# Kernel optimization log

Measured on AMD Instinct MI355X. Metric: run time of the kernel, lower is better.

Reference implementation:

```python
import jax, jax.numpy as jnp
import numpy as np

N_USERS = 100000
N_ITEMS = 50000
N_NODES = N_USERS + N_ITEMS
D = 64
N_LAYERS = 3
POP_BINS = 10
NNZ = 2000000
BATCH = 256
BIAS_SCALE = 1.0


def setup_inputs() -> dict:
    key = jax.random.key(0)
    ks = jax.random.split(key, 16)
    std = 0.01
    inp = {
        "user_emb": jax.random.normal(ks[0], (N_USERS, D), jnp.float32) * std,
        "item_emb": jax.random.normal(ks[1], (N_ITEMS, D), jnp.float32) * std,
        "user_bias": jnp.zeros((N_USERS, 1), jnp.float32),
        "item_bias": jnp.zeros((N_ITEMS, 1), jnp.float32),
        "pop_emb": jax.random.normal(ks[2], (POP_BINS, D), jnp.float32) * std,
        "uW1": jax.random.normal(ks[3], (D, D), jnp.float32) / np.sqrt(D),
        "ub1": jnp.zeros((D,), jnp.float32),
        "uW2": jax.random.normal(ks[4], (D, D), jnp.float32) / np.sqrt(D),
        "ub2": jnp.zeros((D,), jnp.float32),
        "iW1": jax.random.normal(ks[5], (D, D), jnp.float32) / np.sqrt(D),
        "ib1": jnp.zeros((D,), jnp.float32),
        "iW2": jax.random.normal(ks[6], (D, D), jnp.float32) / np.sqrt(D),
        "ib2": jnp.zeros((D,), jnp.float32),
        "gW1": jax.random.normal(ks[7], (2 * D, D), jnp.float32) / np.sqrt(2 * D),
        "gb1": jnp.zeros((D,), jnp.float32),
        "gW2": jax.random.normal(ks[8], (D, 1), jnp.float32) / np.sqrt(D),
        "gb2": jnp.zeros((1,), jnp.float32),
        "adj_vals": jax.random.uniform(ks[9], (NNZ,), jnp.float32),
        "adj_rows": jax.random.randint(ks[10], (NNZ,), 0, N_NODES, jnp.int32),
        "adj_cols": jax.random.randint(ks[11], (NNZ,), 0, N_NODES, jnp.int32),
        "item_pop_bins": jax.random.randint(ks[12], (N_ITEMS,), 0, POP_BINS, jnp.int32),
        "users": jax.random.randint(ks[13], (BATCH,), 0, N_USERS, jnp.int32),
    }
    return inp


def _spmm(vals, rows, cols, E):
    # sparse (N x N) @ E  via gather + segment-sum
    msgs = vals[:, None] * E[cols]          # [nnz, d]
    return jax.ops.segment_sum(msgs, rows, num_segments=N_NODES)


def _mlp2(x, W1, b1, W2, b2):
    return jax.nn.relu(x @ W1 + b1) @ W2 + b2


def reference(user_emb, item_emb, user_bias, item_bias, pop_emb,
              uW1, ub1, uW2, ub2, iW1, ib1, iW2, ib2,
              gW1, gb1, gW2, gb2,
              adj_vals, adj_rows, adj_cols, item_pop_bins, users):
    # ---- computer(): LightGCN propagation with uniform layer weights ----
    emb = jnp.concatenate([user_emb, item_emb], axis=0)   # [N, d]
    w = 1.0 / (N_LAYERS + 1)
    out = emb * w
    cur = emb
    for _ in range(N_LAYERS):
        cur = _spmm(adj_vals, adj_rows, adj_cols, cur)
        out = out + cur * w
    all_users, all_items = out[:N_USERS], out[N_USERS:]

    # ---- popularity-gated item fusion ----
    p_vec = pop_emb[item_pop_bins]                         # [n_items, d]
    gate_in = jnp.concatenate([all_items, p_vec], axis=-1)
    z = jax.nn.sigmoid(_mlp2(gate_in, gW1, gb1, gW2, gb2)) # [n_items, 1]
    items_fused = (1.0 - z) * all_items + z * p_vec

    # ---- two-tower scoring over all items ----
    U = _mlp2(all_users[users], uW1, ub1, uW2, ub2)        # [B, d]
    I = _mlp2(items_fused, iW1, ib1, iW2, ib2)             # [n_items, d]
    scores = U @ I.T                                        # [B, n_items]
    scores = scores + user_bias[users] * BIAS_SCALE + (item_bias.T) * BIAS_SCALE
    return scores
```

## Files before the change

kernel.cpp:

```cpp
#include <hip/hip_runtime.h>
#include <hip/hip_fp16.h>

#define N_USERS 100000
#define N_ITEMS 50000
#define N_NODES 150000
#define D 64
#define NNZ 2000000
#define BATCH 256
#define POP_BINS 10

#define BSH 9
#define NB2 293
#define CAP 8192
#define P1_EPB 4096
#define P1_BLOCKS 489

#define ST_P 130
#define MAXC 7

__global__ __launch_bounds__(256) void k_p1(const int* __restrict__ rows,
                                            const int* __restrict__ cols,
                                            const float* __restrict__ vals,
                                            int* __restrict__ bcur,
                                            uint2* __restrict__ gstage) {
  __shared__ int cnt[NB2];
  __shared__ int gbase[NB2];
  int t = threadIdx.x;
  for (int i = t; i < NB2; i += 256) cnt[i] = 0;
  __syncthreads();
  int base = blockIdx.x * P1_EPB;
  for (int i = 0; i < 16; i++) {
    int e = base + i * 256 + t;
    if (e < NNZ) atomicAdd(&cnt[rows[e] >> BSH], 1);
  }
  __syncthreads();
  for (int i = t; i < NB2; i += 256) {
    int c = cnt[i];
    gbase[i] = c ? atomicAdd(&bcur[i], c) : 0;
    cnt[i] = 0;
  }
  __syncthreads();
  for (int i = 0; i < 16; i++) {
    int e = base + i * 256 + t;
    if (e < NNZ) {
      int r = rows[e];
      int b = r >> BSH;
      int rank = atomicAdd(&cnt[b], 1);
      unsigned key = ((unsigned)(r & 511) << 18) | (unsigned)cols[e];
      gstage[(size_t)b * CAP + gbase[b] + rank] =
          make_uint2(key, __float_as_uint(vals[e]));
    }
  }
}

__global__ __launch_bounds__(256) void k_p2(const int* __restrict__ bcur,
                                            const uint2* __restrict__ gstage,
                                            uint2* __restrict__ epack,
                                            int* __restrict__ rowbeg,
                                            int* __restrict__ rowend,
                                            int* __restrict__ gcursor) {
  __shared__ int cnt[512];
  __shared__ int off[512];
  __shared__ int s[256];
  __shared__ int gbs;
  __shared__ uint2 buf[CAP];
  int b = blockIdx.x, t = threadIdx.x;
  int n = bcur[b];
  const uint2* gs = gstage + (size_t)b * CAP;
  if (t == 0) gbs = atomicAdd(gcursor, n);
  cnt[t] = 0;
  cnt[t + 256] = 0;
  __syncthreads();
  for (int j = t; j < n; j += 256)
    atomicAdd(&cnt[gs[j].x >> 18], 1);
  __syncthreads();
  int c0 = cnt[2 * t], c1 = cnt[2 * t + 1];
  s[t] = c0 + c1;
  __syncthreads();
  for (int o = 1; o < 256; o <<= 1) {
    int x = (t >= o) ? s[t - o] : 0;
    __syncthreads();
    s[t] += x;
    __syncthreads();
  }
  int ex = t ? s[t - 1] : 0;
  off[2 * t] = ex;
  off[2 * t + 1] = ex + c0;
  int base = gbs;
  int gr = (b << BSH) + 2 * t;
  if (gr < N_NODES) { rowbeg[gr] = base + ex; rowend[gr] = base + ex + c0; }
  if (gr + 1 < N_NODES) { rowbeg[gr + 1] = base + ex + c0; rowend[gr + 1] = base + ex + c0 + c1; }
  __syncthreads();
  for (int j = t; j < n; j += 256) {
    uint2 ed = gs[j];
    int lr = ed.x >> 18;
    int pos = atomicAdd(&off[lr], 1);
    buf[pos] = make_uint2(ed.x & 0x3FFFFu, ed.y);
  }
  __syncthreads();
  for (int j = t; j < n; j += 256) epack[base + j] = buf[j];
}

__global__ __launch_bounds__(256) void k_flags(const int* __restrict__ users,
                                               int* __restrict__ uflag,
                                               int* __restrict__ ulist,
                                               int* __restrict__ ucnt) {
  int u = users[threadIdx.x];
  int old = atomicOr(&uflag[u >> 5], 1 << (u & 31));
  if (!((old >> (u & 31)) & 1)) {
    int p = atomicAdd(ucnt, 1);
    ulist[p] = u;
  }
}

__global__ __launch_bounds__(256) void k_cvt(const float* __restrict__ ue,
                                             const float* __restrict__ ie,
                                             __half* __restrict__ Eh) {
  int t = blockIdx.x * 256 + threadIdx.x;
  if (t >= 2400000) return;
  size_t fo = (size_t)t * 4;
  const float* src = (fo < (size_t)N_USERS * 64) ? ue + fo
                                                 : ie + (fo - (size_t)N_USERS * 64);
  float4 v = *(const float4*)src;
  __half2* dst = (__half2*)(Eh + fo);
  dst[0] = __floats2half2_rn(v.x, v.y);
  dst[1] = __floats2half2_rn(v.z, v.w);
}

#define SPMM_DEEP(TBL)                                                        \
  int n = end - beg;                                                          \
  int nc = (n + 3) >> 2;                                                      \
  if (nc > MAXC) nc = MAXC;                                                   \
  uint2 ed[MAXC];                                                             \
  _Pragma("unroll")                                                           \
  for (int c = 0; c < MAXC; c++) {                                            \
    if (c < nc) {                                                             \
      int jj = beg + 4 * c + q;                                               \
      int jc = jj < end ? jj : end - 1;                                       \
      ed[c] = epack[jc];                                                      \
    }                                                                         \
  }                                                                           \
  uint2 rg[MAXC]; float rv[MAXC];                                             \
  _Pragma("unroll")                                                           \
  for (int c = 0; c < MAXC; c++) {                                            \
    if (c < nc) {                                                             \
      int jj = beg + 4 * c + q;                                               \
      rv[c] = (jj < end) ? __uint_as_float(ed[c].y) : 0.f;                    \
      rg[c] = *(const uint2*)(TBL + (size_t)ed[c].x * 64 + 4 * p);            \
    }                                                                         \
  }                                                                           \
  float a0 = 0.f, a1 = 0.f, a2 = 0.f, a3 = 0.f;                               \
  _Pragma("unroll")                                                           \
  for (int c = 0; c < MAXC; c++) {                                            \
    if (c < nc) {                                                             \
      float2 lo = __half22float2(*(const __half2*)&rg[c].x);                  \
      float2 hi = __half22float2(*(const __half2*)&rg[c].y);                  \
      a0 += rv[c] * lo.x; a1 += rv[c] * lo.y;                                 \
      a2 += rv[c] * hi.x; a3 += rv[c] * hi.y;                                 \
    }                                                                         \
  }                                                                           \
  for (int j = beg + 4 * MAXC; j < end; j += 4) {   \
    int jj = j + q;                                                           \
    int jc = jj < end ? jj : end - 1;                                         \
    uint2 e = epack[jc];                                                      \
    float v = (jj < end) ? __uint_as_float(e.y) : 0.f;                        \
    uint2 r = *(const uint2*)(TBL + (size_t)e.x * 64 + 4 * p);                \
    float2 lo = __half22float2(*(const __half2*)&r.x);                        \
    float2 hi = __half22float2(*(const __half2*)&r.y);                        \
    a0 += v * lo.x; a1 += v * lo.y; a2 += v * hi.x; a3 += v * hi.y;           \
  }                                                                           \
  a0 += __shfl_xor(a0, 16, 64); a0 += __shfl_xor(a0, 32, 64);                 \
  a1 += __shfl_xor(a1, 16, 64); a1 += __shfl_xor(a1, 32, 64);                 \
  a2 += __shfl_xor(a2, 16, 64); a2 += __shfl_xor(a2, 32, 64);                 \
  a3 += __shfl_xor(a3, 16, 64); a3 += __shfl_xor(a3, 32, 64);

__global__ __launch_bounds__(256) void k_spmm1(const int* __restrict__ rowbeg,
                                               const int* __restrict__ rowend,
                                               const uint2* __restrict__ epack,
                                               const float* __restrict__ ue,
                                               const float* __restrict__ ie,
                                               const __half* __restrict__ Eh0,
                                               const int* __restrict__ uflag,
                                               __half* __restrict__ EoutH,
                                               float* __restrict__ Oacc) {
  int wave = blockIdx.x * 4 + (threadIdx.x >> 6);
  int row = __builtin_amdgcn_readfirstlane(wave);
  if (row >= N_NODES) return;
  int lane = threadIdx.x & 63;
  int p = lane & 15, q = lane >> 4;
  int beg = rowbeg[row];
  int end = rowend[row];
  SPMM_DEEP(Eh0)
  if (q == 0) {
    __half2* eo = (__half2*)(EoutH + (size_t)row * 64 + 4 * p);
    eo[0] = __floats2half2_rn(a0, a1);
    eo[1] = __floats2half2_rn(a2, a3);
    bool need = (row >= N_USERS) || (((uflag[row >> 5] >> (row & 31)) & 1) != 0);
    if (need) {
      const float* srow = (row < N_USERS) ? ue + (size_t)row * 64
                                          : ie + (size_t)(row - N_USERS) * 64;
      float4 sv = *(const float4*)(srow + 4 * p);
      *(float4*)(Oacc + (size_t)row * 64 + 4 * p) =
          make_float4(0.25f * (sv.x + a0), 0.25f * (sv.y + a1),
                      0.25f * (sv.z + a2), 0.25f * (sv.w + a3));
    }
  }
}

__global__ __launch_bounds__(256) void k_spmm2h(const int* __restrict__ rowbeg,
                                                const int* __restrict__ rowend,
                                                const uint2* __restrict__ epack,
                                                const __half* __restrict__ Ein,
                                                const int* __restrict__ uflag,
                                                __half* __restrict__ EoutH,
                                                float* __restrict__ Oacc) {
  int wave = blockIdx.x * 4 + (threadIdx.x >> 6);
  int row = __builtin_amdgcn_readfirstlane(wave);
  if (row >= N_NODES) return;
  int lane = threadIdx.x & 63;
  int p = lane & 15, q = lane >> 4;
  int beg = rowbeg[row];
  int end = rowend[row];
  SPMM_DEEP(Ein)
  if (q == 0) {
    __half2* eo = (__half2*)(EoutH + (size_t)row * 64 + 4 * p);
    eo[0] = __floats2half2_rn(a0, a1);
    eo[1] = __floats2half2_rn(a2, a3);
    if (row >= N_USERS || (((uflag[row >> 5] >> (row & 31)) & 1) != 0)) {
      float4* op = (float4*)(Oacc + (size_t)row * 64 + 4 * p);
      float4 cur = *op;
      *op = make_float4(cur.x + 0.25f * a0, cur.y + 0.25f * a1,
                        cur.z + 0.25f * a2, cur.w + 0.25f * a3);
    }
  }
}

__global__ __launch_bounds__(256) void k_spmm3h(const int* __restrict__ rowbeg,
                                                const int* __restrict__ rowend,
                                                const uint2* __restrict__ epack,
                                                const __half* __restrict__ Ein,
                                                const int* __restrict__ ulist,
                                                const int* __restrict__ ucnt,
                                                float* __restrict__ Oacc) {
  int w = blockIdx.x * 4 + (threadIdx.x >> 6);
  int row;
  if (w < N_ITEMS) {
    row = N_USERS + w;
  } else {
    int k = w - N_ITEMS;
    if (k >= ucnt[0]) return;
    row = ulist[k];
  }
  row = __builtin_amdgcn_readfirstlane(row);
  int lane = threadIdx.x & 63;
  int p = lane & 15, q = lane >> 4;
  int beg = rowbeg[row];
  int end = rowend[row];
  SPMM_DEEP(Ein)
  if (q == 0) {
    float4* op = (float4*)(Oacc + (size_t)row * 64 + 4 * p);
    float4 cur = *op;
    *op = make_float4(cur.x + 0.25f * a0, cur.y + 0.25f * a1,
                      cur.z + 0.25f * a2, cur.w + 0.25f * a3);
  }
}

__global__ __launch_bounds__(256) void k_pw(const float* __restrict__ pop,
                                            const float* __restrict__ gW1,
                                            const float* __restrict__ iW1,
                                            float* __restrict__ hp,
                                            float* __restrict__ pp1) {
  for (int idx = threadIdx.x; idx < 2 * POP_BINS * 64; idx += 256) {
    int q = idx;
    bool second = q >= POP_BINS * 64;
    if (second) q -= POP_BINS * 64;
    int b = q >> 6, o = q & 63;
    float s = 0.f;
    if (!second) {
      for (int k = 0; k < 64; k++) s += pop[b * 64 + k] * gW1[(64 + k) * 64 + o];
      hp[q] = s;
    } else {
      for (int k = 0; k < 64; k++) s += pop[b * 64 + k] * iW1[k * 64 + o];
      pp1[q] = s;
    }
  }
}

__global__ __launch_bounds__(256) void k_user(const float* __restrict__ Oacc,
                                              const int* __restrict__ users,
                                              const float* __restrict__ ubias,
                                              const float* __restrict__ uW1,
                                              const float* __restrict__ ub1,
                                              const float* __restrict__ uW2,
                                              const float* __restrict__ ub2,
                                              float* __restrict__ Ut) {
  int ub = blockIdx.x * 4 + (threadIdx.x >> 6);
  int lane = threadIdx.x & 63;
  int u = users[ub];
  float x = Oacc[(size_t)u * 64 + lane];
  float h = ub1[lane];
#pragma unroll
  for (int k = 0; k < 64; k++)
    h = fmaf(__shfl(x, k, 64), uW1[k * 64 + lane], h);
  h = h > 0.f ? h : 0.f;
  float o = ub2[lane];
#pragma unroll
  for (int k = 0; k < 64; k++)
    o = fmaf(__shfl(h, k, 64), uW2[k * 64 + lane], o);
  Ut[lane * 256 + ub] = o;
  if (lane == 0) Ut[64 * 256 + ub] = ubias[u];
}

__global__ __launch_bounds__(256) void k_gemm1z(const float* __restrict__ Oacc,
                                                const float* __restrict__ gW1,
                                                const float* __restrict__ iW1,
                                                const int* __restrict__ bins,
                                                const float* __restrict__ hp,
                                                const float* __restrict__ pp1,
                                                const float* __restrict__ gb1,
                                                const float* __restrict__ gW2,
                                                const float* __restrict__ gb2,
                                                const float* __restrict__ ib1,
                                                float* __restrict__ H1) {
  __shared__ float Is[64 * ST_P];
  __shared__ float Bs[64 * 128];
  __shared__ float zp[128][9];
  __shared__ float zs[128];
  int tid = threadIdx.x;
  int i0 = blockIdx.x * 128;
  {
    int c4 = tid & 15, r0 = tid >> 4;
#pragma unroll
    for (int s = 0; s < 8; s++) {
      int r = r0 + s * 16;
      int it = i0 + r;
      float4 v = make_float4(0.f, 0.f, 0.f, 0.f);
      if (it < N_ITEMS) v = *(const float4*)(Oacc + (size_t)(N_USERS + it) * 64 + c4 * 4);
      Is[(c4 * 4 + 0) * ST_P + r] = v.x;
      Is[(c4 * 4 + 1) * ST_P + r] = v.y;
      Is[(c4 * 4 + 2) * ST_P + r] = v.z;
      Is[(c4 * 4 + 3) * ST_P + r] = v.w;
    }
  }
  for (int idx = tid; idx < 64 * 128; idx += 256) {
    int k = idx >> 7, o = idx & 127;
    Bs[idx] = (o < 64) ? gW1[k * 64 + o] : iW1[k * 64 + (o - 64)];
  }
  __syncthreads();
  int tx = tid & 15, ty = tid >> 4;
  float acc[8][8];
#pragma unroll
  for (int a = 0; a < 8; a++)
#pragma unroll
    for (int b = 0; b < 8; b++) acc[a][b] = 0.f;
  const float* ip = Is + tx * 8;
  const float* wp = Bs + ty * 8;
#pragma unroll 2
  for (int k = 0; k < 64; k++) {
    float4 iv0 = *(const float4*)(ip + k * ST_P);
    float4 iv1 = *(const float4*)(ip + k * ST_P + 4);
    float4 wv0 = *(const float4*)(wp + k * 128);
    float4 wv1 = *(const float4*)(wp + k * 128 + 4);
    float iv[8] = {iv0.x, iv0.y, iv0.z, iv0.w, iv1.x, iv1.y, iv1.z, iv1.w};
    float wv[8] = {wv0.x, wv0.y, wv0.z, wv0.w, wv1.x, wv1.y, wv1.z, wv1.w};
#pragma unroll
    for (int a = 0; a < 8; a++)
#pragma unroll
      for (int b = 0; b < 8; b++) acc[a][b] += iv[a] * wv[b];
  }
  int ibase = i0 + tx * 8;
  if (ty < 8) {
    int o0 = ty * 8;
#pragma unroll
    for (int a = 0; a < 8; a++) {
      int it = ibase + a;
      float p = 0.f;
      if (it < N_ITEMS) {
        int bin = bins[it];
        const float* hpr = hp + bin * 64 + o0;
#pragma unroll
        for (int b = 0; b < 8; b++) {
          float g = acc[a][b] + hpr[b] + gb1[o0 + b];
          g = g > 0.f ? g : 0.f;
          p += g * gW2[o0 + b];
        }
      }
      zp[tx * 8 + a][ty] = p;
    }
  }
  __syncthreads();
  if (tid < 128) {
    float s = gb2[0];
#pragma unroll
    for (int k = 0; k < 8; k++) s += zp[tid][k];
    zs[tid] = 1.f / (1.f + expf(-s));
  }
  __syncthreads();
  if (ty >= 8) {
    int o0 = (ty - 8) * 8;
#pragma unroll
    for (int a = 0; a < 8; a++) {
      int it = ibase + a;
      if (it < N_ITEMS) {
        float z = zs[tx * 8 + a];
        int bin = bins[it];
        const float* ppr = pp1 + bin * 64 + o0;
        float h[8];
#pragma unroll
        for (int b = 0; b < 8; b++) {
          float v = (1.f - z) * acc[a][b] + z * ppr[b] + ib1[o0 + b];
          h[b] = v > 0.f ? v : 0.f;
        }
        *(float4*)(H1 + (size_t)it * 64 + o0) = make_float4(h[0], h[1], h[2], h[3]);
        *(float4*)(H1 + (size_t)it * 64 + o0 + 4) = make_float4(h[4], h[5], h[6], h[7]);
      }
    }
  }
}

__global__ __launch_bounds__(256) void k_gemm2(const float* __restrict__ H1,
                                               const float* __restrict__ iW2,
                                               const float* __restrict__ ib2,
                                               float* __restrict__ I) {
  __shared__ float Is[64 * ST_P];
  __shared__ float Bs[64 * 64];
  int tid = threadIdx.x;
  int i0 = blockIdx.x * 128;
  {
    int c4 = tid & 15, r0 = tid >> 4;
#pragma unroll
    for (int s = 0; s < 8; s++) {
      int r = r0 + s * 16;
      int it = i0 + r;
      float4 v = make_float4(0.f, 0.f, 0.f, 0.f);
      if (it < N_ITEMS) v = *(const float4*)(H1 + (size_t)it * 64 + c4 * 4);
      Is[(c4 * 4 + 0) * ST_P + r] = v.x;
      Is[(c4 * 4 + 1) * ST_P + r] = v.y;
      Is[(c4 * 4 + 2) * ST_P + r] = v.z;
      Is[(c4 * 4 + 3) * ST_P + r] = v.w;
    }
  }
  for (int idx = tid; idx < 64 * 64; idx += 256) Bs[idx] = iW2[idx];
  __syncthreads();
  int tx = tid & 15, ty = tid >> 4;
  float acc[8][4];
#pragma unroll
  for (int a = 0; a < 8; a++)
#pragma unroll
    for (int b = 0; b < 4; b++) acc[a][b] = 0.f;
  const float* ip = Is + tx * 8;
  const float* wp = Bs + ty * 4;
#pragma unroll 2
  for (int k = 0; k < 64; k++) {
    float4 iv0 = *(const float4*)(ip + k * ST_P);
    float4 iv1 = *(const float4*)(ip + k * ST_P + 4);
    float4 wv = *(const float4*)(wp + k * 64);
    float iv[8] = {iv0.x, iv0.y, iv0.z, iv0.w, iv1.x, iv1.y, iv1.z, iv1.w};
    float wvv[4] = {wv.x, wv.y, wv.z, wv.w};
#pragma unroll
    for (int a = 0; a < 8; a++)
#pragma unroll
      for (int b = 0; b < 4; b++) acc[a][b] += iv[a] * wvv[b];
  }
  int ibase = i0 + tx * 8;
  int oc = ty * 4;
  float b0 = ib2[oc], b1 = ib2[oc + 1], b2 = ib2[oc + 2], b3 = ib2[oc + 3];
#pragma unroll
  for (int a = 0; a < 8; a++) {
    int it = ibase + a;
    if (it < N_ITEMS) {
      float4 s0 = make_float4(acc[a][0] + b0, acc[a][1] + b1,
                              acc[a][2] + b2, acc[a][3] + b3);
      *(float4*)(I + (size_t)it * 64 + oc) = s0;
    }
  }
}

__global__ __launch_bounds__(256) void k_scores(const float* __restrict__ I,
                                                const float* __restrict__ Ut,
                                                const float* __restrict__ item_bias,
                                                float* __restrict__ out) {
  __shared__ float Is[64 * ST_P];
  __shared__ float Us[64 * 128];
  int tid = threadIdx.x;
  int i0 = blockIdx.x * 128;
  int ubase = blockIdx.y * 128;
  {
    int c4 = tid & 15, r0 = tid >> 4;
#pragma unroll
    for (int s = 0; s < 8; s++) {
      int r = r0 + s * 16;
      int it = i0 + r;
      float4 v = make_float4(0.f, 0.f, 0.f, 0.f);
      if (it < N_ITEMS) v = *(const float4*)(I + (size_t)it * 64 + c4 * 4);
      Is[(c4 * 4 + 0) * ST_P + r] = v.x;
      Is[(c4 * 4 + 1) * ST_P + r] = v.y;
      Is[(c4 * 4 + 2) * ST_P + r] = v.z;
      Is[(c4 * 4 + 3) * ST_P + r] = v.w;
    }
  }
  {
    int u4 = tid & 31, k0 = tid >> 5;
#pragma unroll
    for (int s = 0; s < 8; s++) {
      int k = k0 + s * 8;
      float4 v = *(const float4*)(Ut + k * 256 + ubase + u4 * 4);
      *(float4*)(Us + k * 128 + u4 * 4) = v;
    }
  }
  __syncthreads();
  int tx = tid & 15;
  int ty = tid >> 4;
  float acc[8][8];
#pragma unroll
  for (int a = 0; a < 8; a++)
#pragma unroll
    for (int b = 0; b < 8; b++) acc[a][b] = 0.f;
  const float* ip = Is + tx * 8;
  const float* up = Us + ty * 8;
#pragma unroll 2
  for (int k = 0; k < 64; k++) {
    float4 iv0 = *(const float4*)(ip + k * ST_P);
    float4 iv1 = *(const float4*)(ip + k * ST_P + 4);
    float4 uv0 = *(const float4*)(up + k * 128);
    float4 uv1 = *(const float4*)(up + k * 128 + 4);
    float iv[8] = {iv0.x, iv0.y, iv0.z, iv0.w, iv1.x, iv1.y, iv1.z, iv1.w};
    float uv[8] = {uv0.x, uv0.y, uv0.z, uv0.w, uv1.x, uv1.y, uv1.z, uv1.w};
#pragma unroll
    for (int a = 0; a < 8; a++)
#pragma unroll
      for (int b = 0; b < 8; b++) acc[a][b] += iv[a] * uv[b];
  }
  int ibase = i0 + tx * 8;
  float ib[8];
#pragma unroll
  for (int a = 0; a < 8; a++)
    ib[a] = (ibase + a < N_ITEMS) ? item_bias[ibase + a] : 0.f;
#pragma unroll
  for (int bb = 0; bb < 8; bb++) {
    int bu = ubase + ty * 8 + bb;
    float ubias = Ut[64 * 256 + bu];
    float* orow = out + (size_t)bu * N_ITEMS + ibase;
    if (ibase + 7 < N_ITEMS) {
      float4 s0 = make_float4(acc[0][bb] + ubias + ib[0], acc[1][bb] + ubias + ib[1],
                              acc[2][bb] + ubias + ib[2], acc[3][bb] + ubias + ib[3]);
      float4 s1 = make_float4(acc[4][bb] + ubias + ib[4], acc[5][bb] + ubias + ib[5],
                              acc[6][bb] + ubias + ib[6], acc[7][bb] + ubias + ib[7]);
      *(float4*)orow = s0;
      *(float4*)(orow + 4) = s1;
    } else {
#pragma unroll
      for (int a = 0; a < 8; a++)
        if (ibase + a < N_ITEMS) orow[a] = acc[a][bb] + ubias + ib[a];
    }
  }
}

extern "C" void kernel_launch(void* const* d_in, const int* in_sizes, int n_in,
                              void* d_out, int out_size, void* d_ws, size_t ws_size,
                              hipStream_t stream) {
  const float* user_emb  = (const float*)d_in[0];
  const float* item_emb  = (const float*)d_in[1];
  const float* user_bias = (const float*)d_in[2];
  const float* item_bias = (const float*)d_in[3];
  const float* pop_emb   = (const float*)d_in[4];
  const float* uW1 = (const float*)d_in[5];
  const float* ub1 = (const float*)d_in[6];
  const float* uW2 = (const float*)d_in[7];
  const float* ub2 = (const float*)d_in[8];
  const float* iW1 = (const float*)d_in[9];
  const float* ib1 = (const float*)d_in[10];
  const float* iW2 = (const float*)d_in[11];
  const float* ib2 = (const float*)d_in[12];
  const float* gW1 = (const float*)d_in[13];
  const float* gb1 = (const float*)d_in[14];
  const float* gW2 = (const float*)d_in[15];
  const float* gb2 = (const float*)d_in[16];
  const float* adj_vals = (const float*)d_in[17];
  const int* adj_rows = (const int*)d_in[18];
  const int* adj_cols = (const int*)d_in[19];
  const int* bins  = (const int*)d_in[20];
  const int* users = (const int*)d_in[21];
  float* out = (float*)d_out;

  float* ws = (float*)d_ws;
  float* Oacc = ws;
  float* bufA = ws + 9600000;
  float* bufB = ws + 19200000;
  uint2* epack = (uint2*)(ws + 28800000);
  int* rowbeg = (int*)(ws + 32800000);
  int* rowend = (int*)(ws + 32950000);
  int* uflag  = (int*)(ws + 33100000);
  int* ucnt   = (int*)(ws + 33103125);
  int* ulist  = (int*)(ws + 33103130);
  float* Ut   = ws + 33104000;
  float* hp   = ws + 33121000;
  float* pp1  = ws + 33122000;
  int* bcur   = (int*)(ws + 33123000);
  int* gcursor = (int*)(ws + 33123293);
  uint2* gstage = (uint2*)bufB;
  __half* Eh0 = (__half*)bufA;
  __half* E1h = (__half*)(bufA + 4800000);
  __half* E2h = (__half*)bufB;
  float* H1 = bufA + 6400000;
  float* I  = bufB;

  hipMemsetAsync(bcur, 0, 294 * sizeof(int), stream);
  hipMemsetAsync(uflag, 0, 3126 * sizeof(int), stream);
  k_cvt<<<9375, 256, 0, stream>>>(user_emb, item_emb, Eh0);
  k_p1<<<P1_BLOCKS, 256, 0, stream>>>(adj_rows, adj_cols, adj_vals, bcur, gstage);
  k_p2<<<NB2, 256, 0, stream>>>(bcur, gstage, epack, rowbeg, rowend, gcursor);
  k_flags<<<1, 256, 0, stream>>>(users, uflag, ulist, ucnt);

  k_spmm1<<<37500, 256, 0, stream>>>(rowbeg, rowend, epack, user_emb, item_emb, Eh0, uflag, E1h, Oacc);
  k_spmm2h<<<37500, 256, 0, stream>>>(rowbeg, rowend, epack, E1h, uflag, E2h, Oacc);
  k_spmm3h<<<12564, 256, 0, stream>>>(rowbeg, rowend, epack, E2h, ulist, ucnt, Oacc);

  k_pw<<<1, 256, 0, stream>>>(pop_emb, gW1, iW1, hp, pp1);
  k_user<<<64, 256, 0, stream>>>(Oacc, users, user_bias, uW1, ub1, uW2, ub2, Ut);
  k_gemm1z<<<391, 256, 0, stream>>>(Oacc, gW1, iW1, bins, hp, pp1, gb1, gW2, gb2, ib1, H1);
  k_gemm2<<<391, 256, 0, stream>>>(H1, iW2, ib2, I);
  k_scores<<<dim3(391, 2), 256, 0, stream>>>(I, Ut, item_bias, out);
}
```

Measured before the change: 505.6 us.

## Fuse small kernels, merge item MLP GEMMs, simplify SpMM gather loop

Folds the user-flag kernel into an extra block of the bucket-sort kernel and the pop-weight kernel into an extra block of the fp16 conversion kernel. It also merges the two item-MLP GEMMs so H1 stays in shared memory instead of going through global memory. The scores kernel now loops over both user halves per block rather than using a 2D grid. The SpMM gather replaces the deep register-prefetch loop with a simpler 2-way unrolled loop, and the workspace layout is rearranged so a single memset clears the flags and counters. Together these cut launch overhead and global traffic, at the risk of less memory-level parallelism in the SpMM and lower parallelism in the scores kernel.

```diff
diff --git a/kernel.cpp b/kernel.cpp
--- a/kernel.cpp
+++ b/kernel.cpp
@@ -16,7 +16,6 @@
 #define P1_BLOCKS 489
 
 #define ST_P 130
-#define MAXC 7
 
 __global__ __launch_bounds__(256) void k_p1(const int* __restrict__ rows,
                                             const int* __restrict__ cols,
@@ -58,13 +57,26 @@
                                             uint2* __restrict__ epack,
                                             int* __restrict__ rowbeg,
                                             int* __restrict__ rowend,
-                                            int* __restrict__ gcursor) {
+                                            int* __restrict__ gcursor,
+                                            const int* __restrict__ users,
+                                            int* __restrict__ uflag,
+                                            int* __restrict__ ulist,
+                                            int* __restrict__ ucnt) {
+  int b = blockIdx.x, t = threadIdx.x;
+  if (b == NB2) {
+    int u = users[t];
+    int old = atomicOr(&uflag[u >> 5], 1 << (u & 31));
+    if (!((old >> (u & 31)) & 1)) {
+      int p = atomicAdd(ucnt, 1);
+      ulist[p] = u;
+    }
+    return;
+  }
   __shared__ int cnt[512];
   __shared__ int off[512];
   __shared__ int s[256];
   __shared__ int gbs;
   __shared__ uint2 buf[CAP];
-  int b = blockIdx.x, t = threadIdx.x;
   int n = bcur[b];
   const uint2* gs = gstage + (size_t)b * CAP;
   if (t == 0) gbs = atomicAdd(gcursor, n);
@@ -101,23 +113,33 @@
   for (int j = t; j < n; j += 256) epack[base + j] = buf[j];
 }
 
-__global__ __launch_bounds__(256) void k_flags(const int* __restrict__ users,
-                                               int* __restrict__ uflag,
-                                               int* __restrict__ ulist,
-                                               int* __restrict__ ucnt) {
-  int u = users[threadIdx.x];
-  int old = atomicOr(&uflag[u >> 5], 1 << (u & 31));
-  if (!((old >> (u & 31)) & 1)) {
-    int p = atomicAdd(ucnt, 1);
-    ulist[p] = u;
-  }
-}
-
-__global__ __launch_bounds__(256) void k_cvt(const float* __restrict__ ue,
-                                             const float* __restrict__ ie,
-                                             __half* __restrict__ Eh) {
-  int t = blockIdx.x * 256 + threadIdx.x;
-  if (t >= 2400000) return;
+__global__ __launch_bounds__(256) void k_prep(const float* __restrict__ ue,
+                                              const float* __restrict__ ie,
+                                              __half* __restrict__ Eh,
+                                              const float* __restrict__ pop,
+                                              const float* __restrict__ gW1,
+                                              const float* __restrict__ iW1,
+                                              float* __restrict__ hp,
+                                              float* __restrict__ pp1) {
+  int b = blockIdx.x;
+  if (b == 9375) {
+    for (int idx = threadIdx.x; idx < 2 * POP_BINS * 64; idx += 256) {
+      int q = idx;
+      bool second = q >= POP_BINS * 64;
+      if (second) q -= POP_BINS * 64;
+      int bb = q >> 6, o = q & 63;
+      float s = 0.f;
+      if (!second) {
+        for (int k = 0; k < 64; k++) s += pop[bb * 64 + k] * gW1[(64 + k) * 64 + o];
+        hp[q] = s;
+      } else {
+        for (int k = 0; k < 64; k++) s += pop[bb * 64 + k] * iW1[k * 64 + o];
+        pp1[q] = s;
+      }
+    }
+    return;
+  }
+  int t = b * 256 + threadIdx.x;
   size_t fo = (size_t)t * 4;
   const float* src = (fo < (size_t)N_USERS * 64) ? ue + fo
                                                  : ie + (fo - (size_t)N_USERS * 64);
@@ -127,41 +149,25 @@
   dst[1] = __floats2half2_rn(v.z, v.w);
 }
 
-#define SPMM_DEEP(TBL)                                                        \
-  int n = end - beg;                                                          \
-  int nc = (n + 3) >> 2;                                                      \
-  if (nc > MAXC) nc = MAXC;                                                   \
-  uint2 ed[MAXC];                                                             \
-  _Pragma("unroll")                                                           \
-  for (int c = 0; c < MAXC; c++) {                                            \
-    if (c < nc) {                                                             \
-      int jj = beg + 4 * c + q;                                               \
-      int jc = jj < end ? jj : end - 1;                                       \
-      ed[c] = epack[jc];                                                      \
-    }                                                                         \
+#define SPMM_QW_BODY(TBL)                                                     \
+  float a0 = 0.f, a1 = 0.f, a2 = 0.f, a3 = 0.f;                               \
+  int j = beg;                                                                \
+  for (; j + 7 < end; j += 8) {                                               \
+    uint2 ea = epack[j + q];                                                  \
+    uint2 eb = epack[j + 4 + q];                                              \
+    uint2 ra = *(const uint2*)(TBL + (size_t)ea.x * 64 + 4 * p);              \
+    uint2 rb = *(const uint2*)(TBL + (size_t)eb.x * 64 + 4 * p);              \
+    float va = __uint_as_float(ea.y), vb = __uint_as_float(eb.y);             \
+    float2 la = __half22float2(*(const __half2*)&ra.x);                       \
+    float2 ha = __half22float2(*(const __half2*)&ra.y);                       \
+    float2 lb = __half22float2(*(const __half2*)&rb.x);                       \
+    float2 hb = __half22float2(*(const __half2*)&rb.y);                       \
+    a0 += va * la.x; a1 += va * la.y; a2 += va * ha.x; a3 += va * ha.y;       \
+    a0 += vb * lb.x; a1 += vb * lb.y; a2 += vb * hb.x; a3 += vb * hb.y;       \
   }                                                                           \
-  uint2 rg[MAXC]; float rv[MAXC];                                             \
-  _Pragma("unroll")                                                           \
-  for (int c = 0; c < MAXC; c++) {                                            \
-    if (c < nc) {                                                             \
-      int jj = beg + 4 * c + q;                                               \
-      rv[c] = (jj < end) ? __uint_as_float(ed[c].y) : 0.f;                    \
-      rg[c] = *(const uint2*)(TBL + (size_t)ed[c].x * 64 + 4 * p);            \
-    }                                                                         \
-  }                                                                           \
-  float a0 = 0.f, a1 = 0.f, a2 = 0.f, a3 = 0.f;                               \
-  _Pragma("unroll")                                                           \
-  for (int c = 0; c < MAXC; c++) {                                            \
-    if (c < nc) {                                                             \
-      float2 lo = __half22float2(*(const __half2*)&rg[c].x);                  \
-      float2 hi = __half22float2(*(const __half2*)&rg[c].y);                  \
-      a0 += rv[c] * lo.x; a1 += rv[c] * lo.y;                                 \
-      a2 += rv[c] * hi.x; a3 += rv[c] * hi.y;                                 \
-    }                                                                         \
-  }                                                                           \
-  for (int j = beg + 4 * MAXC; j < end; j += 4) {   \
+  for (; j < end; j += 4) {                                                   \
     int jj = j + q;                                                           \
-    int jc = jj < end ? jj : end - 1;                                         \
+    int jc = (jj < end) ? jj : end - 1;                                       \
     uint2 e = epack[jc];                                                      \
     float v = (jj < end) ? __uint_as_float(e.y) : 0.f;                        \
     uint2 r = *(const uint2*)(TBL + (size_t)e.x * 64 + 4 * p);                \
@@ -190,7 +196,7 @@
   int p = lane & 15, q = lane >> 4;
   int beg = rowbeg[row];
   int end = rowend[row];
-  SPMM_DEEP(Eh0)
+  SPMM_QW_BODY(Eh0)
   if (q == 0) {
     __half2* eo = (__half2*)(EoutH + (size_t)row * 64 + 4 * p);
     eo[0] = __floats2half2_rn(a0, a1);
@@ -221,7 +227,7 @@
   int p = lane & 15, q = lane >> 4;
   int beg = rowbeg[row];
   int end = rowend[row];
-  SPMM_DEEP(Ein)
+  SPMM_QW_BODY(Ein)
   if (q == 0) {
     __half2* eo = (__half2*)(EoutH + (size_t)row * 64 + 4 * p);
     eo[0] = __floats2half2_rn(a0, a1);
@@ -256,33 +262,12 @@
   int p = lane & 15, q = lane >> 4;
   int beg = rowbeg[row];
   int end = rowend[row];
-  SPMM_DEEP(Ein)
+  SPMM_QW_BODY(Ein)
   if (q == 0) {
     float4* op = (float4*)(Oacc + (size_t)row * 64 + 4 * p);
     float4 cur = *op;
     *op = make_float4(cur.x + 0.25f * a0, cur.y + 0.25f * a1,
                       cur.z + 0.25f * a2, cur.w + 0.25f * a3);
-  }
-}
-
-__global__ __launch_bounds__(256) void k_pw(const float* __restrict__ pop,
-                                            const float* __restrict__ gW1,
-                                            const float* __restrict__ iW1,
-                                            float* __restrict__ hp,
-                                            float* __restrict__ pp1) {
-  for (int idx = threadIdx.x; idx < 2 * POP_BINS * 64; idx += 256) {
-    int q = idx;
-    bool second = q >= POP_BINS * 64;
-    if (second) q -= POP_BINS * 64;
-    int b = q >> 6, o = q & 63;
-    float s = 0.f;
-    if (!second) {
-      for (int k = 0; k < 64; k++) s += pop[b * 64 + k] * gW1[(64 + k) * 64 + o];
-      hp[q] = s;
-    } else {
-      for (int k = 0; k < 64; k++) s += pop[b * 64 + k] * iW1[k * 64 + o];
-      pp1[q] = s;
-    }
   }
 }
 
@@ -311,7 +296,7 @@
   if (lane == 0) Ut[64 * 256 + ub] = ubias[u];
 }
 
-__global__ __launch_bounds__(256) void k_gemm1z(const float* __restrict__ Oacc,
+__global__ __launch_bounds__(256) void k_gemm12(const float* __restrict__ Oacc,
                                                 const float* __restrict__ gW1,
                                                 const float* __restrict__ iW1,
                                                 const int* __restrict__ bins,
@@ -321,7 +306,9 @@
                                                 const float* __restrict__ gW2,
                                                 const float* __restrict__ gb2,
                                                 const float* __restrict__ ib1,
-                                                float* __restrict__ H1) {
+                                                const float* __restrict__ iW2,
+                                                const float* __restrict__ ib2,
+                                                float* __restrict__ I) {
   __shared__ float Is[64 * ST_P];
   __shared__ float Bs[64 * 128];
   __shared__ float zp[128][9];
@@ -353,20 +340,22 @@
   for (int a = 0; a < 8; a++)
 #pragma unroll
     for (int b = 0; b < 8; b++) acc[a][b] = 0.f;
-  const float* ip = Is + tx * 8;
-  const float* wp = Bs + ty * 8;
+  {
+    const float* ip = Is + tx * 8;
+    const float* wp = Bs + ty * 8;
 #pragma unroll 2
-  for (int k = 0; k < 64; k++) {
-    float4 iv0 = *(const float4*)(ip + k * ST_P);
-    float4 iv1 = *(const float4*)(ip + k * ST_P + 4);
-    float4 wv0 = *(const float4*)(wp + k * 128);
-    float4 wv1 = *(const float4*)(wp + k * 128 + 4);
-    float iv[8] = {iv0.x, iv0.y, iv0.z, iv0.w, iv1.x, iv1.y, iv1.z, iv1.w};
-    float wv[8] = {wv0.x, wv0.y, wv0.z, wv0.w, wv1.x, wv1.y, wv1.z, wv1.w};
-#pragma unroll
-    for (int a = 0; a < 8; a++)
-#pragma unroll
-      for (int b = 0; b < 8; b++) acc[a][b] += iv[a] * wv[b];
+    for (int k = 0; k < 64; k++) {
+      float4 iv0 = *(const float4*)(ip + k * ST_P);
+      float4 iv1 = *(const float4*)(ip + k * ST_P + 4);
+      float4 wv0 = *(const float4*)(wp + k * 128);
+      float4 wv1 = *(const float4*)(wp + k * 128 + 4);
+      float iv[8] = {iv0.x, iv0.y, iv0.z, iv0.w, iv1.x, iv1.y, iv1.z, iv1.w};
+      float wv[8] = {wv0.x, wv0.y, wv0.z, wv0.w, wv1.x, wv1.y, wv1.z, wv1.w};
+#pragma unroll
+      for (int a = 0; a < 8; a++)
+#pragma unroll
+        for (int b = 0; b < 8; b++) acc[a][b] += iv[a] * wv[b];
+    }
   }
   int ibase = i0 + tx * 8;
   if (ty < 8) {
@@ -401,76 +390,48 @@
 #pragma unroll
     for (int a = 0; a < 8; a++) {
       int it = ibase + a;
-      if (it < N_ITEMS) {
-        float z = zs[tx * 8 + a];
-        int bin = bins[it];
-        const float* ppr = pp1 + bin * 64 + o0;
-        float h[8];
-#pragma unroll
-        for (int b = 0; b < 8; b++) {
-          float v = (1.f - z) * acc[a][b] + z * ppr[b] + ib1[o0 + b];
-          h[b] = v > 0.f ? v : 0.f;
-        }
-        *(float4*)(H1 + (size_t)it * 64 + o0) = make_float4(h[0], h[1], h[2], h[3]);
-        *(float4*)(H1 + (size_t)it * 64 + o0 + 4) = make_float4(h[4], h[5], h[6], h[7]);
+      int item = tx * 8 + a;
+      float z = zs[item];
+      int bin = (it < N_ITEMS) ? bins[it] : 0;
+      const float* ppr = pp1 + bin * 64 + o0;
+#pragma unroll
+      for (int b = 0; b < 8; b++) {
+        float v = (1.f - z) * acc[a][b] + z * ppr[b] + ib1[o0 + b];
+        Is[(o0 + b) * ST_P + item] = v > 0.f ? v : 0.f;
       }
     }
   }
-}
-
-__global__ __launch_bounds__(256) void k_gemm2(const float* __restrict__ H1,
-                                               const float* __restrict__ iW2,
-                                               const float* __restrict__ ib2,
-                                               float* __restrict__ I) {
-  __shared__ float Is[64 * ST_P];
-  __shared__ float Bs[64 * 64];
-  int tid = threadIdx.x;
-  int i0 = blockIdx.x * 128;
+  for (int idx = tid; idx < 64 * 64; idx += 256) Bs[idx] = iW2[idx];
+  __syncthreads();
+  float acc2[8][4];
+#pragma unroll
+  for (int a = 0; a < 8; a++)
+#pragma unroll
+    for (int b = 0; b < 4; b++) acc2[a][b] = 0.f;
   {
-    int c4 = tid & 15, r0 = tid >> 4;
-#pragma unroll
-    for (int s = 0; s < 8; s++) {
-      int r = r0 + s * 16;
-      int it = i0 + r;
-      float4 v = make_float4(0.f, 0.f, 0.f, 0.f);
-      if (it < N_ITEMS) v = *(const float4*)(H1 + (size_t)it * 64 + c4 * 4);
-      Is[(c4 * 4 + 0) * ST_P + r] = v.x;
-      Is[(c4 * 4 + 1) * ST_P + r] = v.y;
-      Is[(c4 * 4 + 2) * ST_P + r] = v.z;
-      Is[(c4 * 4 + 3) * ST_P + r] = v.w;
-    }
-  }
-  for (int idx = tid; idx < 64 * 64; idx += 256) Bs[idx] = iW2[idx];
-  __syncthreads();
-  int tx = tid & 15, ty = tid >> 4;
-  float acc[8][4];
-#pragma unroll
-  for (int a = 0; a < 8; a++)
-#pragma unroll
-    for (int b = 0; b < 4; b++) acc[a][b] = 0.f;
-  const float* ip = Is + tx * 8;
-  const float* wp = Bs + ty * 4;
+    const float* ip = Is + tx * 8;
+    const float* wp = Bs + ty * 4;
 #pragma unroll 2
-  for (int k = 0; k < 64; k++) {
-    float4 iv0 = *(const float4*)(ip + k * ST_P);
-    float4 iv1 = *(const float4*)(ip + k * ST_P + 4);
-    float4 wv = *(const float4*)(wp + k * 64);
-    float iv[8] = {iv0.x, iv0.y, iv0.z, iv0.w, iv1.x, iv1.y, iv1.z, iv1.w};
-    float wvv[4] = {wv.x, wv.y, wv.z, wv.w};
-#pragma unroll
-    for (int a = 0; a < 8; a++)
-#pragma unroll
-      for (int b = 0; b < 4; b++) acc[a][b] += iv[a] * wvv[b];
-  }
-  int ibase = i0 + tx * 8;
+    for (int k = 0; k < 64; k++) {
+      float4 iv0 = *(const float4*)(ip + k * ST_P);
+      float4 iv1 = *(const float4*)(ip + k * ST_P + 4);
+      float4 wv = *(const float4*)(wp + k * 64);
+      float iv[8] = {iv0.x, iv0.y, iv0.z, iv0.w, iv1.x, iv1.y, iv1.z, iv1.w};
+      float wvv[4] = {wv.x, wv.y, wv.z, wv.w};
+#pragma unroll
+      for (int a = 0; a < 8; a++)
+#pragma unroll
+        for (int b = 0; b < 4; b++) acc2[a][b] += iv[a] * wvv[b];
+    }
+  }
   int oc = ty * 4;
   float b0 = ib2[oc], b1 = ib2[oc + 1], b2 = ib2[oc + 2], b3 = ib2[oc + 3];
 #pragma unroll
   for (int a = 0; a < 8; a++) {
     int it = ibase + a;
     if (it < N_ITEMS) {
-      float4 s0 = make_float4(acc[a][0] + b0, acc[a][1] + b1,
-                              acc[a][2] + b2, acc[a][3] + b3);
+      float4 s0 = make_float4(acc2[a][0] + b0, acc2[a][1] + b1,
+                              acc2[a][2] + b2, acc2[a][3] + b3);
       *(float4*)(I + (size_t)it * 64 + oc) = s0;
     }
   }
@@ -484,7 +445,6 @@
   __shared__ float Us[64 * 128];
   int tid = threadIdx.x;
   int i0 = blockIdx.x * 128;
-  int ubase = blockIdx.y * 128;
   {
     int c4 = tid & 15, r0 = tid >> 4;
 #pragma unroll
@@ -499,59 +459,63 @@
       Is[(c4 * 4 + 3) * ST_P + r] = v.w;
     }
   }
-  {
-    int u4 = tid & 31, k0 = tid >> 5;
-#pragma unroll
-    for (int s = 0; s < 8; s++) {
-      int k = k0 + s * 8;
-      float4 v = *(const float4*)(Ut + k * 256 + ubase + u4 * 4);
-      *(float4*)(Us + k * 128 + u4 * 4) = v;
-    }
-  }
-  __syncthreads();
   int tx = tid & 15;
   int ty = tid >> 4;
-  float acc[8][8];
-#pragma unroll
-  for (int a = 0; a < 8; a++)
-#pragma unroll
-    for (int b = 0; b < 8; b++) acc[a][b] = 0.f;
-  const float* ip = Is + tx * 8;
-  const float* up = Us + ty * 8;
-#pragma unroll 2
-  for (int k = 0; k < 64; k++) {
-    float4 iv0 = *(const float4*)(ip + k * ST_P);
-    float4 iv1 = *(const float4*)(ip + k * ST_P + 4);
-    float4 uv0 = *(const float4*)(up + k * 128);
-    float4 uv1 = *(const float4*)(up + k * 128 + 4);
-    float iv[8] = {iv0.x, iv0.y, iv0.z, iv0.w, iv1.x, iv1.y, iv1.z, iv1.w};
-    float uv[8] = {uv0.x, uv0.y, uv0.z, uv0.w, uv1.x, uv1.y, uv1.z, uv1.w};
-#pragma unroll
-    for (int a = 0; a < 8; a++)
-#pragma unroll
-      for (int b = 0; b < 8; b++) acc[a][b] += iv[a] * uv[b];
-  }
   int ibase = i0 + tx * 8;
   float ib[8];
 #pragma unroll
   for (int a = 0; a < 8; a++)
     ib[a] = (ibase + a < N_ITEMS) ? item_bias[ibase + a] : 0.f;
-#pragma unroll
-  for (int bb = 0; bb < 8; bb++) {
-    int bu = ubase + ty * 8 + bb;
-    float ubias = Ut[64 * 256 + bu];
-    float* orow = out + (size_t)bu * N_ITEMS + ibase;
-    if (ibase + 7 < N_ITEMS) {
-      float4 s0 = make_float4(acc[0][bb] + ubias + ib[0], acc[1][bb] + ubias + ib[1],
-                              acc[2][bb] + ubias + ib[2], acc[3][bb] + ubias + ib[3]);
-      float4 s1 = make_float4(acc[4][bb] + ubias + ib[4], acc[5][bb] + ubias + ib[5],
-                              acc[6][bb] + ubias + ib[6], acc[7][bb] + ubias + ib[7]);
-      *(float4*)orow = s0;
-      *(float4*)(orow + 4) = s1;
-    } else {
+  for (int uh = 0; uh < 2; uh++) {
+    int ubase = uh * 128;
+    if (uh) __syncthreads();
+    {
+      int u4 = tid & 31, k0 = tid >> 5;
+#pragma unroll
+      for (int s = 0; s < 8; s++) {
+        int k = k0 + s * 8;
+        float4 v = *(const float4*)(Ut + k * 256 + ubase + u4 * 4);
+        *(float4*)(Us + k * 128 + u4 * 4) = v;
+      }
+    }
+    __syncthreads();
+    float acc[8][8];
+#pragma unroll
+    for (int a = 0; a < 8; a++)
+#pragma unroll
+      for (int b = 0; b < 8; b++) acc[a][b] = 0.f;
+    const float* ip = Is + tx * 8;
+    const float* up = Us + ty * 8;
+#pragma unroll 2
+    for (int k = 0; k < 64; k++) {
+      float4 iv0 = *(const float4*)(ip + k * ST_P);
+      float4 iv1 = *(const float4*)(ip + k * ST_P + 4);
+      float4 uv0 = *(const float4*)(up + k * 128);
+      float4 uv1 = *(const float4*)(up + k * 128 + 4);
+      float iv[8] = {iv0.x, iv0.y, iv0.z, iv0.w, iv1.x, iv1.y, iv1.z, iv1.w};
+      float uv[8] = {uv0.x, uv0.y, uv0.z, uv0.w, uv1.x, uv1.y, uv1.z, uv1.w};
 #pragma unroll
       for (int a = 0; a < 8; a++)
-        if (ibase + a < N_ITEMS) orow[a] = acc[a][bb] + ubias + ib[a];
+#pragma unroll
+        for (int b = 0; b < 8; b++) acc[a][b] += iv[a] * uv[b];
+    }
+#pragma unroll
+    for (int bb = 0; bb < 8; bb++) {
+      int bu = ubase + ty * 8 + bb;
+      float ubias = Ut[64 * 256 + bu];
+      float* orow = out + (size_t)bu * N_ITEMS + ibase;
+      if (ibase + 7 < N_ITEMS) {
+        float4 s0 = make_float4(acc[0][bb] + ubias + ib[0], acc[1][bb] + ubias + ib[1],
+                                acc[2][bb] + ubias + ib[2], acc[3][bb] + ubias + ib[3]);
+        float4 s1 = make_float4(acc[4][bb] + ubias + ib[4], acc[5][bb] + ubias + ib[5],
+                                acc[6][bb] + ubias + ib[6], acc[7][bb] + ubias + ib[7]);
+        *(float4*)orow = s0;
+        *(float4*)(orow + 4) = s1;
+      } else {
+#pragma unroll
+        for (int a = 0; a < 8; a++)
+          if (ibase + a < N_ITEMS) orow[a] = acc[a][bb] + ubias + ib[a];
+      }
     }
   }
 }
@@ -590,35 +554,33 @@
   uint2* epack = (uint2*)(ws + 28800000);
   int* rowbeg = (int*)(ws + 32800000);
   int* rowend = (int*)(ws + 32950000);
-  int* uflag  = (int*)(ws + 33100000);
-  int* ucnt   = (int*)(ws + 33103125);
-  int* ulist  = (int*)(ws + 33103130);
+  int* uflag   = (int*)(ws + 33100000);
+  int* ucnt    = (int*)(ws + 33103125);
+  int* bcur    = (int*)(ws + 33103126);
+  int* gcursor = (int*)(ws + 33103419);
+  int* ulist   = (int*)(ws + 33103420);
   float* Ut   = ws + 33104000;
   float* hp   = ws + 33121000;
   float* pp1  = ws + 33122000;
-  int* bcur   = (int*)(ws + 33123000);
-  int* gcursor = (int*)(ws + 33123293);
   uint2* gstage = (uint2*)bufB;
   __half* Eh0 = (__half*)bufA;
   __half* E1h = (__half*)(bufA + 4800000);
   __half* E2h = (__half*)bufB;
-  float* H1 = bufA + 6400000;
   float* I  = bufB;
 
-  hipMemsetAsync(bcur, 0, 294 * sizeof(int), stream);
-  hipMemsetAsync(uflag, 0, 3126 * sizeof(int), stream);
-  k_cvt<<<9375, 256, 0, stream>>>(user_emb, item_emb, Eh0);
+  hipMemsetAsync(uflag, 0, 3680 * sizeof(int), stream);
+  k_prep<<<9376, 256, 0, stream>>>(user_emb, item_emb, Eh0, pop_emb, gW1, iW1, hp, pp1);
   k_p1<<<P1_BLOCKS, 256, 0, stream>>>(adj_rows, adj_cols, adj_vals, bcur, gstage);
-  k_p2<<<NB2, 256, 0, stream>>>(bcur, gstage, epack, rowbeg, rowend, gcursor);
-  k_flags<<<1, 256, 0, stream>>>(users, uflag, ulist, ucnt);
-
-  k_spmm1<<<37500, 256, 0, stream>>>(rowbeg, rowend, epack, user_emb, item_emb, Eh0, uflag, E1h, Oacc);
+  k_p2<<<NB2 + 1, 256, 0, stream>>>(bcur, gstage, epack, rowbeg, rowend, gcursor,
+                                    users, uflag, ulist, ucnt);
+
+  k_spmm1<<<37500, 256, 0, stream>>>(rowbeg, rowend, epack, user_emb, item_emb,
+                                     Eh0, uflag, E1h, Oacc);
   k_spmm2h<<<37500, 256, 0, stream>>>(rowbeg, rowend, epack, E1h, uflag, E2h, Oacc);
   k_spmm3h<<<12564, 256, 0, stream>>>(rowbeg, rowend, epack, E2h, ulist, ucnt, Oacc);
 
-  k_pw<<<1, 256, 0, stream>>>(pop_emb, gW1, iW1, hp, pp1);
   k_user<<<64, 256, 0, stream>>>(Oacc, users, user_bias, uW1, ub1, uW2, ub2, Ut);
-  k_gemm1z<<<391, 256, 0, stream>>>(Oacc, gW1, iW1, bins, hp, pp1, gb1, gW2, gb2, ib1, H1);
-  k_gemm2<<<391, 256, 0, stream>>>(H1, iW2, ib2, I);
-  k_scores<<<dim3(391, 2), 256, 0, stream>>>(I, Ut, item_bias, out);
-}
+  k_gemm12<<<391, 256, 0, stream>>>(Oacc, gW1, iW1, bins, hp, pp1, gb1, gW2, gb2,
+                                    ib1, iW2, ib2, I);
+  k_scores<<<391, 256, 0, stream>>>(I, Ut, item_bias, out);
+}
```

New measurement: 476.4 us. 1.06x faster.
